# Kernel optimization log

Hardware: AMD Instinct MI355X
Metric: run time of the kernel (lower is better)

## Reference

```python
import jax, jax.numpy as jnp
import numpy as np

EPS = 1e-5

def _bn_train(x, gamma, beta):
    # BatchNorm2d in training mode: batch stats over (N,H,W), biased variance
    mean = jnp.mean(x, axis=(0, 2, 3), keepdims=True)
    var = jnp.mean((x - mean) ** 2, axis=(0, 2, 3), keepdims=True)
    xn = (x - mean) / jnp.sqrt(var + EPS)
    return xn * gamma[None, :, None, None] + beta[None, :, None, None]

def _bin_act(x):
    # forward: sign(x); backward: grad of clamp(x,-1,1) (STE)
    c = jnp.clip(x, -1.0, 1.0)
    return jax.lax.stop_gradient(jnp.sign(x) - c) + c

def _bin_conv(x, w_flat, out_chn, in_chn, k=3, stride=1, padding=1):
    w = w_flat.reshape(out_chn, in_chn, k, k)
    scale = jax.lax.stop_gradient(jnp.mean(jnp.abs(w), axis=(1, 2, 3), keepdims=True))
    cw = jnp.clip(w, -1.0, 1.0)
    bw = jax.lax.stop_gradient(scale * jnp.sign(w) - cw) + cw
    return jax.lax.conv_general_dilated(
        x, bw, window_strides=(stride, stride),
        padding=[(padding, padding), (padding, padding)],
        dimension_numbers=('NCHW', 'OIHW', 'NCHW'))

def _prelu(x, a):
    return jnp.where(x >= 0, x, a * x)

def setup_inputs() -> dict:
    key = jax.random.key(0)
    ks = jax.random.split(key, 4)
    C = 128
    x = jax.random.normal(ks[0], (64, C, 56, 56), dtype=jnp.float32)
    # HardBinaryConv stores weights as (n,1); init small, mixed-sign
    w1 = (jax.random.uniform(ks[1], (C * C * 9, 1), dtype=jnp.float32) - 0.5) * 0.002
    w2 = (jax.random.uniform(ks[2], (C * C * 9, 1), dtype=jnp.float32) - 0.5) * 0.002
    ones = jnp.ones((C,), jnp.float32)
    zeros = jnp.zeros((C,), jnp.float32)
    a = jnp.float32(0.25)
    return {
        'x': x,
        'bn1_g': ones, 'bn1_b': zeros,
        'w1': w1, 'prelu1_a': a,
        'bn2_g': ones, 'bn2_b': zeros,
        'w2': w2, 'prelu2_a': a,
        'bn3_g': ones, 'bn3_b': zeros,
        'prelu3_a': a,
    }

def reference(x, bn1_g, bn1_b, w1, prelu1_a, bn2_g, bn2_b, w2, prelu2_a, bn3_g, bn3_b, prelu3_a):
    C = x.shape[1]
    out = _bn_train(x, bn1_g, bn1_b)
    out = _bin_act(out)
    out = _prelu(_bin_conv(out, w1, C, C), prelu1_a)
    out = _bn_train(out, bn2_g, bn2_b)
    out = _bin_act(out)
    out = _bin_conv(out, w2, C, C)
    out = _prelu(out, prelu2_a)
    out = _bn_train(out, bn3_g, bn3_b)
    out = out + x  # identity shortcut (stride=1, in_planes==planes)
    out = _prelu(out, prelu3_a)
    return out
```

## Files before the change

### kernel.cpp

```cpp
#include <hip/hip_runtime.h>
#include <hip/hip_bf16.h>

typedef __attribute__((ext_vector_type(8))) short short8;
typedef __attribute__((ext_vector_type(4))) int i32x4;

#define HW     3136
#define M_TOT  200704
#define NSTEP  18
#define NBLK   784

__device__ __forceinline__ void gload_lds16(const void* g, void* l) {
    __builtin_amdgcn_global_load_lds(
        (const __attribute__((address_space(1))) void*)g,
        (__attribute__((address_space(3))) void*)l, 16, 0, 0);
}

__global__ __launch_bounds__(256) void wsign_kernel(const float* __restrict__ w1,
                                                    const float* __restrict__ w2,
                                                    char* __restrict__ ws1,
                                                    char* __restrict__ ws2) {
    int i = blockIdx.x * 256 + threadIdx.x;
    const float* w = w1;
    char* wsz = ws1;
    if (i >= 147456) { i -= 147456; w = w2; wsz = ws2; }
    int e = i & 15, l = (i >> 4) & 63, f = (i >> 10) & 7, s = i >> 13;
    int cout = f * 16 + (l & 15);
    int k = s * 64 + (l >> 4) * 16 + e;
    int tap = k >> 7, cin = k & 127;
    float v = w[(cout * 128 + cin) * 9 + tap];
    wsz[i] = v > 0.f ? (char)1 : (v < 0.f ? (char)-1 : (char)0);
}

__global__ __launch_bounds__(256) void wscale_kernel(const float* __restrict__ w1,
                                                     const float* __restrict__ w2,
                                                     float* __restrict__ scale1,
                                                     float* __restrict__ scale2) {
    int o = blockIdx.x;
    const float* w = w1;
    float* scale = scale1;
    if (o >= 128) { o -= 128; w = w2; scale = scale2; }
    int t = threadIdx.x;
    float s = 0.f;
    for (int i = t; i < 1152; i += 256) s += fabsf(w[o * 1152 + i]);
    __shared__ float r1[256];
    r1[t] = s; __syncthreads();
    for (int off = 128; off > 0; off >>= 1) {
        if (t < off) r1[t] += r1[t + off];
        __syncthreads();
    }
    if (t == 0) scale[o] = r1[0] * (1.f / 1152.f);
}

__global__ __launch_bounds__(256) void stats_nchw_kernel(const float* __restrict__ x,
                                                         float* __restrict__ psum,
                                                         float* __restrict__ psq) {
    int bid = blockIdx.x;
    int n = bid >> 7, c = bid & 127;
    const float* p = x + (n * 128 + c) * HW;
    int t = threadIdx.x;
    float s = 0.f, q = 0.f;
    for (int i = t; i < HW; i += 256) { float v = p[i]; s += v; q += v * v; }
    __shared__ float r1[256], r2[256];
    r1[t] = s; r2[t] = q; __syncthreads();
    for (int off = 128; off > 0; off >>= 1) {
        if (t < off) { r1[t] += r1[t + off]; r2[t] += r2[t + off]; }
        __syncthreads();
    }
    if (t == 0) { psum[c * 64 + n] = r1[0]; psq[c * 64 + n] = r2[0]; }
}

__global__ void finalize_kernel(const float* __restrict__ psum, const float* __restrict__ psq,
                                int P, float* __restrict__ mean, float* __restrict__ rstd) {
    int c = threadIdx.x;
    if (c >= 128) return;
    float s = 0.f, q = 0.f;
    for (int j = 0; j < P; ++j) { s += psum[c * P + j]; q += psq[c * P + j]; }
    const float invN = 1.f / 200704.f;
    float m = s * invN;
    float var = q * invN - m * m;
    mean[c] = m;
    rstd[c] = 1.f / sqrtf(var + 1e-5f);
}

__global__ __launch_bounds__(256) void finalizeB_kernel(const float* __restrict__ psumB,
                                                        const float* __restrict__ psqB,
                                                        float* __restrict__ mean,
                                                        float* __restrict__ rstd) {
    int c = blockIdx.x, t = threadIdx.x;
    float s = 0.f, q = 0.f;
    for (int j = t; j < NBLK; j += 256) { s += psumB[j * 128 + c]; q += psqB[j * 128 + c]; }
    __shared__ float r1[256], r2[256];
    r1[t] = s; r2[t] = q; __syncthreads();
    for (int off = 128; off > 0; off >>= 1) {
        if (t < off) { r1[t] += r1[t + off]; r2[t] += r2[t + off]; }
        __syncthreads();
    }
    if (t == 0) {
        const float invN = 1.f / 200704.f;
        float m = r1[0] * invN;
        float var = r2[0] * invN - m * m;
        mean[c] = m;
        rstd[c] = 1.f / sqrtf(var + 1e-5f);
    }
}

__global__ __launch_bounds__(256) void act1_kernel(const float* __restrict__ x,
        const float* __restrict__ mean, const float* __restrict__ rstd,
        const float* __restrict__ g, const float* __restrict__ b,
        char* __restrict__ apad) {
    __shared__ float row[128 * 57];
    int blk = blockIdx.x;
    int n = blk / 58, hp = blk - n * 58;
    char* o = apad + (n * 58 + hp) * 58 * 128;
    int t = threadIdx.x;
    if (hp == 0 || hp == 57) {
        for (int i4 = t; i4 < 58 * 32; i4 += 256)
            *(char4*)(o + i4 * 4) = make_char4(0, 0, 0, 0);
        return;
    }
    const float* src = x + n * (128 * HW) + (hp - 1) * 56;
    for (int i = t; i < 128 * 56; i += 256) {
        int c = i / 56, w = i - c * 56;
        row[c * 57 + w] = src[c * HW + w];
    }
    __syncthreads();
    for (int i4 = t; i4 < 58 * 32; i4 += 256) {
        int wp = i4 >> 5;
        int c0 = (i4 & 31) * 4;
        char q[4] = {0, 0, 0, 0};
        if (wp >= 1 && wp <= 56) {
#pragma unroll
            for (int k = 0; k < 4; ++k) {
                int c = c0 + k;
                float xn = (row[c * 57 + wp - 1] - mean[c]) * rstd[c] * g[c] + b[c];
                q[k] = xn > 0.f ? 1 : (xn < 0.f ? -1 : 0);
            }
        }
        *(char4*)(o + wp * 128 + c0) = make_char4(q[0], q[1], q[2], q[3]);
    }
}

__global__ __launch_bounds__(256) void act2_kernel(const short* __restrict__ p1,
        const float* __restrict__ scale1, const float* __restrict__ a1ptr,
        const float* __restrict__ mean, const float* __restrict__ rstd,
        const float* __restrict__ g, const float* __restrict__ b,
        char* __restrict__ apad) {
    __shared__ float row[128 * 57];
    int blk = blockIdx.x;
    int n = blk / 58, hp = blk - n * 58;
    char* o = apad + (n * 58 + hp) * 58 * 128;
    int t = threadIdx.x;
    if (hp == 0 || hp == 57) {
        for (int i4 = t; i4 < 58 * 32; i4 += 256)
            *(char4*)(o + i4 * 4) = make_char4(0, 0, 0, 0);
        return;
    }
    float a1 = a1ptr[0];
    const short* src = p1 + n * HW + (hp - 1) * 56;
    for (int i = t; i < 128 * 56; i += 256) {
        int c = i / 56, w = i - c * 56;
        float v = scale1[c] * (float)src[(size_t)c * M_TOT + w];
        row[c * 57 + w] = v >= 0.f ? v : a1 * v;
    }
    __syncthreads();
    for (int i4 = t; i4 < 58 * 32; i4 += 256) {
        int wp = i4 >> 5;
        int c0 = (i4 & 31) * 4;
        char q[4] = {0, 0, 0, 0};
        if (wp >= 1 && wp <= 56) {
#pragma unroll
            for (int k = 0; k < 4; ++k) {
                int c = c0 + k;
                float xn = (row[c * 57 + wp - 1] - mean[c]) * rstd[c] * g[c] + b[c];
                q[k] = xn > 0.f ? 1 : (xn < 0.f ? -1 : 0);
            }
        }
        *(char4*)(o + wp * 128 + c0) = make_char4(q[0], q[1], q[2], q[3]);
    }
}

__global__ __launch_bounds__(256, 2) void conv_kernel(
        const char* __restrict__ apad,
        const char* __restrict__ wswz,
        const float* __restrict__ scale,
        const float* __restrict__ aptr,
        short* __restrict__ obuf,
        float* __restrict__ psumB,
        float* __restrict__ psqB) {
    __shared__ __align__(1024) char lds[3][24576];

    const int tid = threadIdx.x;
    const int lane = tid & 63;
    const int wid = tid >> 6;
    const int l15 = lane & 15;
    const int lq = lane >> 4;
    const int wr = wid >> 1;
    const int wc = wid & 1;

    int bid = blockIdx.x;
    int mblk = (bid & 7) * 98 + (bid >> 3);
    const int m0 = mblk * 256;

    const char* bsrc[4];
#pragma unroll
    for (int j = 0; j < 4; ++j) {
        int jt = j >> 1, jj = j & 1;
        int m = m0 + jt * 128 + (jj * 4 + wid) * 16 + l15;
        int n = m / HW;
        int r = m - n * HW;
        int h = r / 56;
        int w = r - h * 56;
        bsrc[j] = apad + (((n * 58 + h) * 58 + w) * 128 + lq * 16);
    }

    i32x4 acc[4][8];
#pragma unroll
    for (int i = 0; i < 4; ++i)
#pragma unroll
        for (int j = 0; j < 8; ++j)
            acc[i][j] = (i32x4){0, 0, 0, 0};

    auto stage = [&](int s, int buf) {
        int tap = s >> 1;
        int dh = tap / 3;
        int dw = tap - dh * 3;
        int toff = (dh * 58 + dw) * 128 + (s & 1) * 64;
        const char* wsrc = wswz + s * 8192 + tid * 16;
        gload_lds16(wsrc,        lds[buf] + wid * 1024);
        gload_lds16(wsrc + 4096, lds[buf] + 4096 + wid * 1024);
        gload_lds16(bsrc[0] + toff, lds[buf] + 8192 + wid * 1024);
        gload_lds16(bsrc[1] + toff, lds[buf] + 12288 + wid * 1024);
        gload_lds16(bsrc[2] + toff, lds[buf] + 16384 + wid * 1024);
        gload_lds16(bsrc[3] + toff, lds[buf] + 20480 + wid * 1024);
    };

    stage(0, 0);
    stage(1, 1);

    for (int s = 0; s < NSTEP; ++s) {
        if (s + 1 < NSTEP) asm volatile("s_waitcnt vmcnt(6)" ::: "memory");
        else               asm volatile("s_waitcnt vmcnt(0)" ::: "memory");
        __builtin_amdgcn_s_barrier();
        __builtin_amdgcn_sched_barrier(0);
        if (s + 2 < NSTEP) stage(s + 2, (s + 2) % 3);

        const char* buf = lds[s % 3];
        i32x4 af[4], bf[8];
#pragma unroll
        for (int ci = 0; ci < 4; ++ci)
            af[ci] = *(const i32x4*)(buf + (wr * 4 + ci) * 1024 + lane * 16);
#pragma unroll
        for (int t2 = 0; t2 < 2; ++t2)
#pragma unroll
            for (int mi = 0; mi < 4; ++mi)
                bf[t2 * 4 + mi] = *(const i32x4*)(buf + 8192 + t2 * 8192 +
                                                  (wc * 4 + mi) * 1024 + lane * 16);
#pragma unroll
        for (int ci = 0; ci < 4; ++ci)
#pragma unroll
            for (int j = 0; j < 8; ++j)
                acc[ci][j] = __builtin_amdgcn_mfma_i32_16x16x64_i8(
                    af[ci], bf[j], acc[ci][j], 0, 0, 0);
    }

    float alpha = aptr[0];
    float* partS = (float*)&lds[0][0];
    float* partQ = (float*)&lds[0][1024];
#pragma unroll
    for (int ci = 0; ci < 4; ++ci) {
        int cb = wr * 64 + ci * 16 + lq * 4;
#pragma unroll
        for (int r = 0; r < 4; ++r) {
            float sc = scale[cb + r];
            float s = 0.f, q = 0.f;
#pragma unroll
            for (int t2 = 0; t2 < 2; ++t2) {
                int mb = m0 + t2 * 128 + wc * 64 + l15;
                short* op = obuf + (size_t)(cb + r) * M_TOT + mb;
#pragma unroll
                for (int mi = 0; mi < 4; ++mi) {
                    int iv = acc[ci][t2 * 4 + mi][r];
                    float v = (float)iv * sc;
                    float pv = v >= 0.f ? v : alpha * v;
                    op[mi * 16] = (short)iv;
                    s += pv; q += pv * pv;
                }
            }
#pragma unroll
            for (int msk = 1; msk <= 8; msk <<= 1) {
                s += __shfl_xor(s, msk, 64);
                q += __shfl_xor(q, msk, 64);
            }
            if (l15 == 0) { partS[wc * 128 + cb + r] = s; partQ[wc * 128 + cb + r] = q; }
        }
    }
    __syncthreads();
    if (tid < 128) {
        psumB[bid * 128 + tid] = partS[tid] + partS[128 + tid];
        psqB [bid * 128 + tid] = partQ[tid] + partQ[128 + tid];
    }
}

__global__ __launch_bounds__(256) void final_kernel(const short* __restrict__ p2,
        const float* __restrict__ scale2, const float* __restrict__ a2ptr,
        const float* __restrict__ x,
        const float* __restrict__ mean, const float* __restrict__ rstd,
        const float* __restrict__ g, const float* __restrict__ b,
        const float* __restrict__ a3ptr, float* __restrict__ out) {
    int bid = blockIdx.x;
    int n = bid >> 7, c = bid & 127;
    float sc = scale2[c], a2 = a2ptr[0];
    float m = mean[c], r = rstd[c], gg = g[c], bb = b[c], a3 = a3ptr[0];
    const short* pp = p2 + (size_t)c * M_TOT + n * HW;
    const float* xx = x + (n * 128 + c) * HW;
    float* oo = out + (n * 128 + c) * HW;
    int t = threadIdx.x;
    for (int i8 = t; i8 < 392; i8 += 256) {
        short8 v = *(const short8*)(pp + i8 * 8);
        float4 x0 = *(const float4*)(xx + i8 * 8);
        float4 x1 = *(const float4*)(xx + i8 * 8 + 4);
        float o[8];
#pragma unroll
        for (int k = 0; k < 8; ++k) {
            float pv = (float)v[k] * sc;
            pv = pv >= 0.f ? pv : a2 * pv;
            float xv = (k < 4) ? ((const float*)&x0)[k] : ((const float*)&x1)[k - 4];
            float val = (pv - m) * r * gg + bb + xv;
            o[k] = val >= 0.f ? val : a3 * val;
        }
        *(float4*)(oo + i8 * 8)     = make_float4(o[0], o[1], o[2], o[3]);
        *(float4*)(oo + i8 * 8 + 4) = make_float4(o[4], o[5], o[6], o[7]);
    }
}

extern "C" void kernel_launch(void* const* d_in, const int* in_sizes, int n_in,
                              void* d_out, int out_size, void* d_ws, size_t ws_size,
                              hipStream_t stream) {
    const float* x  = (const float*)d_in[0];
    const float* g1 = (const float*)d_in[1];
    const float* b1 = (const float*)d_in[2];
    const float* w1 = (const float*)d_in[3];
    const float* a1 = (const float*)d_in[4];
    const float* g2 = (const float*)d_in[5];
    const float* b2 = (const float*)d_in[6];
    const float* w2 = (const float*)d_in[7];
    const float* a2 = (const float*)d_in[8];
    const float* g3 = (const float*)d_in[9];
    const float* b3 = (const float*)d_in[10];
    const float* a3 = (const float*)d_in[11];
    float* out = (float*)d_out;
    char* ws = (char*)d_ws;

    float* scale1 = (float*)(ws);
    float* scale2 = (float*)(ws + 512);
    float* mean1  = (float*)(ws + 1024);
    float* rstd1  = (float*)(ws + 1536);
    float* mean2  = (float*)(ws + 2048);
    float* rstd2  = (float*)(ws + 2560);
    float* mean3  = (float*)(ws + 3072);
    float* rstd3  = (float*)(ws + 3584);
    float* psum   = (float*)(ws + 4096);
    float* psq    = (float*)(ws + 36864);
    float* psumB  = (float*)(ws + 69632);
    float* psqB   = (float*)(ws + 872448);
    char* wswz1   = (char*)(ws + 1675264);
    char* wswz2   = (char*)(ws + 1822720);
    char* apad8   = (char*)(ws + 1970176);
    short* buf2s  = (short*)(ws + 29528064);
    short* buf1s  = (short*)out;

    wscale_kernel<<<256, 256, 0, stream>>>(w1, w2, scale1, scale2);
    wsign_kernel<<<1152, 256, 0, stream>>>(w1, w2, wswz1, wswz2);

    stats_nchw_kernel<<<8192, 256, 0, stream>>>(x, psum, psq);
    finalize_kernel<<<1, 128, 0, stream>>>(psum, psq, 64, mean1, rstd1);
    act1_kernel<<<3712, 256, 0, stream>>>(x, mean1, rstd1, g1, b1, apad8);
    conv_kernel<<<NBLK, 256, 0, stream>>>(apad8, wswz1, scale1, a1, buf1s, psumB, psqB);

    finalizeB_kernel<<<128, 256, 0, stream>>>(psumB, psqB, mean2, rstd2);
    act2_kernel<<<3712, 256, 0, stream>>>(buf1s, scale1, a1, mean2, rstd2, g2, b2, apad8);
    conv_kernel<<<NBLK, 256, 0, stream>>>(apad8, wswz2, scale2, a2, buf2s, psumB, psqB);

    finalizeB_kernel<<<128, 256, 0, stream>>>(psumB, psqB, mean3, rstd3);
    final_kernel<<<8192, 256, 0, stream>>>(buf2s, scale2, a2, x, mean3, rstd3, g3, b3, a3, out);
}
```

Measured before the change: 274.4 us.

## Stage input row slab once in LDS with XOR swizzle for conv

The conv kernel now loads a whole padded 6-row input slab (4 output rows plus halo) into LDS once per block with an XOR swizzle. It then builds all 9 tap operands from that slab instead of re-fetching activation tiles from global memory at every K step. Tiles change from 256 output pixels to 224 (4 rows of 56), giving 896 blocks, and only the weights stay triple-buffered. This cuts redundant global/L2 traffic for the overlapping 3x3 windows. In exchange LDS use per block grows to about 68KB, which may limit occupancy, and the slab load is not overlapped with compute.

```diff
diff --git a/kernel.cpp b/kernel.cpp
--- a/kernel.cpp
+++ b/kernel.cpp
@@ -7,7 +7,8 @@
 #define HW     3136
 #define M_TOT  200704
 #define NSTEP  18
-#define NBLK   784
+#define NBLK   896
+#define SLABB  44544
 
 __device__ __forceinline__ void gload_lds16(const void* g, void* l) {
     __builtin_amdgcn_global_load_lds(
@@ -187,7 +188,7 @@
         short* __restrict__ obuf,
         float* __restrict__ psumB,
         float* __restrict__ psqB) {
-    __shared__ __align__(1024) char lds[3][24576];
+    __shared__ __align__(1024) char lds[SLABB + 3 * 8192];
 
     const int tid = threadIdx.x;
     const int lane = tid & 63;
@@ -198,93 +199,105 @@
     const int wc = wid & 1;
 
     int bid = blockIdx.x;
-    int mblk = (bid & 7) * 98 + (bid >> 3);
-    const int m0 = mblk * 256;
-
-    const char* bsrc[4];
-#pragma unroll
-    for (int j = 0; j < 4; ++j) {
-        int jt = j >> 1, jj = j & 1;
-        int m = m0 + jt * 128 + (jj * 4 + wid) * 16 + l15;
-        int n = m / HW;
-        int r = m - n * HW;
-        int h = r / 56;
-        int w = r - h * 56;
-        bsrc[j] = apad + (((n * 58 + h) * 58 + w) * 128 + lq * 16);
-    }
-
-    i32x4 acc[4][8];
+    int mblk = (bid & 7) * 112 + (bid >> 3);
+    const int n = mblk / 14;
+    const int hg = mblk - n * 14;
+    const int m0 = n * HW + hg * 224;
+
+    const char* slabsrc = apad + (size_t)(n * 58 + hg * 4) * 58 * 128;
+    char* slab = lds;
+    char* Abuf = lds + SLABB;
+
+    {
+#pragma unroll
+        for (int i = 0; i < 11; ++i) {
+            int gbyte = i * 4096 + tid * 16;
+            if (i < 10 || gbyte < SLABB) {
+                int r = gbyte >> 7;
+                int cp = (gbyte >> 4) & 7;
+                int wp = r % 58;
+                gload_lds16(slabsrc + (gbyte & ~127) + ((cp ^ (wp & 7)) << 4),
+                            slab + i * 4096 + wid * 1024);
+            }
+        }
+    }
+
+    int Pm[7], Wm[7];
+#pragma unroll
+    for (int mi = 0; mi < 7; ++mi) {
+        int mloc = wc * 112 + mi * 16 + l15;
+        int ho = mloc / 56;
+        int w = mloc - ho * 56;
+        Pm[mi] = (ho * 58 + w) * 128;
+        Wm[mi] = w;
+    }
+
+    auto stageA = [&](int s, int buf) {
+        const char* wsrc = wswz + s * 8192 + tid * 16;
+        gload_lds16(wsrc,        Abuf + buf * 8192 + wid * 1024);
+        gload_lds16(wsrc + 4096, Abuf + buf * 8192 + 4096 + wid * 1024);
+    };
+
+    i32x4 acc[4][7];
 #pragma unroll
     for (int i = 0; i < 4; ++i)
 #pragma unroll
-        for (int j = 0; j < 8; ++j)
+        for (int j = 0; j < 7; ++j)
             acc[i][j] = (i32x4){0, 0, 0, 0};
 
-    auto stage = [&](int s, int buf) {
+    stageA(0, 0);
+    stageA(1, 1);
+
+    for (int s = 0; s < NSTEP; ++s) {
+        if (s + 1 < NSTEP) asm volatile("s_waitcnt vmcnt(2)" ::: "memory");
+        else               asm volatile("s_waitcnt vmcnt(0)" ::: "memory");
+        __builtin_amdgcn_s_barrier();
+        __builtin_amdgcn_sched_barrier(0);
+        if (s + 2 < NSTEP) stageA(s + 2, (s + 2) % 3);
+
         int tap = s >> 1;
         int dh = tap / 3;
         int dw = tap - dh * 3;
-        int toff = (dh * 58 + dw) * 128 + (s & 1) * 64;
-        const char* wsrc = wswz + s * 8192 + tid * 16;
-        gload_lds16(wsrc,        lds[buf] + wid * 1024);
-        gload_lds16(wsrc + 4096, lds[buf] + 4096 + wid * 1024);
-        gload_lds16(bsrc[0] + toff, lds[buf] + 8192 + wid * 1024);
-        gload_lds16(bsrc[1] + toff, lds[buf] + 12288 + wid * 1024);
-        gload_lds16(bsrc[2] + toff, lds[buf] + 16384 + wid * 1024);
-        gload_lds16(bsrc[3] + toff, lds[buf] + 20480 + wid * 1024);
-    };
-
-    stage(0, 0);
-    stage(1, 1);
-
-    for (int s = 0; s < NSTEP; ++s) {
-        if (s + 1 < NSTEP) asm volatile("s_waitcnt vmcnt(6)" ::: "memory");
-        else               asm volatile("s_waitcnt vmcnt(0)" ::: "memory");
-        __builtin_amdgcn_s_barrier();
-        __builtin_amdgcn_sched_barrier(0);
-        if (s + 2 < NSTEP) stage(s + 2, (s + 2) % 3);
-
-        const char* buf = lds[s % 3];
-        i32x4 af[4], bf[8];
+        int Q = (dh * 58 + dw) * 128;
+        int s4 = (s & 1) * 4;
+        int c16 = s4 + lq;
+
+        const char* abuf = Abuf + (s % 3) * 8192;
+        i32x4 af[4], bf[7];
 #pragma unroll
         for (int ci = 0; ci < 4; ++ci)
-            af[ci] = *(const i32x4*)(buf + (wr * 4 + ci) * 1024 + lane * 16);
-#pragma unroll
-        for (int t2 = 0; t2 < 2; ++t2)
-#pragma unroll
-            for (int mi = 0; mi < 4; ++mi)
-                bf[t2 * 4 + mi] = *(const i32x4*)(buf + 8192 + t2 * 8192 +
-                                                  (wc * 4 + mi) * 1024 + lane * 16);
+            af[ci] = *(const i32x4*)(abuf + (wr * 4 + ci) * 1024 + lane * 16);
+#pragma unroll
+        for (int mi = 0; mi < 7; ++mi) {
+            int wxd = (Wm[mi] + dw) & 7;
+            bf[mi] = *(const i32x4*)(slab + Pm[mi] + Q + ((c16 ^ wxd) << 4));
+        }
 #pragma unroll
         for (int ci = 0; ci < 4; ++ci)
 #pragma unroll
-            for (int j = 0; j < 8; ++j)
-                acc[ci][j] = __builtin_amdgcn_mfma_i32_16x16x64_i8(
-                    af[ci], bf[j], acc[ci][j], 0, 0, 0);
+            for (int mi = 0; mi < 7; ++mi)
+                acc[ci][mi] = __builtin_amdgcn_mfma_i32_16x16x64_i8(
+                    af[ci], bf[mi], acc[ci][mi], 0, 0, 0);
     }
 
     float alpha = aptr[0];
-    float* partS = (float*)&lds[0][0];
-    float* partQ = (float*)&lds[0][1024];
+    float* partS = (float*)Abuf;
+    float* partQ = (float*)(Abuf + 1024);
 #pragma unroll
     for (int ci = 0; ci < 4; ++ci) {
         int cb = wr * 64 + ci * 16 + lq * 4;
 #pragma unroll
         for (int r = 0; r < 4; ++r) {
             float sc = scale[cb + r];
+            short* op = obuf + (size_t)(cb + r) * M_TOT + m0 + wc * 112 + l15;
             float s = 0.f, q = 0.f;
 #pragma unroll
-            for (int t2 = 0; t2 < 2; ++t2) {
-                int mb = m0 + t2 * 128 + wc * 64 + l15;
-                short* op = obuf + (size_t)(cb + r) * M_TOT + mb;
-#pragma unroll
-                for (int mi = 0; mi < 4; ++mi) {
-                    int iv = acc[ci][t2 * 4 + mi][r];
-                    float v = (float)iv * sc;
-                    float pv = v >= 0.f ? v : alpha * v;
-                    op[mi * 16] = (short)iv;
-                    s += pv; q += pv * pv;
-                }
+            for (int mi = 0; mi < 7; ++mi) {
+                int iv = acc[ci][mi][r];
+                float v = (float)iv * sc;
+                float pv = v >= 0.f ? v : alpha * v;
+                op[mi * 16] = (short)iv;
+                s += pv; q += pv * pv;
             }
 #pragma unroll
             for (int msk = 1; msk <= 8; msk <<= 1) {
```

Result: faster. 247.4 us (-9.8%).
